# Kernel tuning notes

Hardware: AMD Instinct MI355X
Metric: run time of the kernel (lower is better)

## Reference

```python
import jax, jax.numpy as jnp
import numpy as np

B, N = 2, 65536
GX, GY, NH = 480, 360, 32          # grid_size
FEA_DIM, OUT_DIM, MAX_PT = 9, 512, 256
HW = GX * GY


def setup_inputs() -> dict:
    key = jax.random.key(0)
    ks = jax.random.split(key, 24)
    def rn(k, shape, scale):
        return jax.random.normal(k, shape, jnp.float32) * scale
    d = {}
    d['pt_fea'] = jax.random.normal(ks[0], (B, N, FEA_DIM), jnp.float32)
    d['xy_ind'] = jax.random.randint(ks[1], (B, N, 2), 0, 360)
    # eval-mode BatchNorm1d folded into per-channel scale/shift
    for i, c in enumerate([FEA_DIM, 64, 128, 256]):
        d[f's{i}'] = 1.0 + rn(ks[2 + 2 * i], (c,), 0.05)
        d[f't{i}'] = rn(ks[3 + 2 * i], (c,), 0.05)
    for i, (cin, cout) in enumerate([(FEA_DIM, 64), (64, 128), (128, 256), (256, OUT_DIM)], 1):
        d[f'W{i}'] = rn(ks[9 + 2 * i], (cin, cout), 1.0 / np.sqrt(cin))
        d[f'b{i}'] = rn(ks[10 + 2 * i], (cout,), 0.02)
    d['Wc'] = rn(ks[20], (OUT_DIM, NH), 1.0 / np.sqrt(OUT_DIM))
    d['bc'] = rn(ks[21], (NH,), 0.02)
    return d


def _ranks(lin):
    # within-voxel rank of each point (== grp_range_torch(...)[argsort(argsort(unq_inv))])
    n = lin.shape[0]
    order = jnp.argsort(lin, stable=True)
    sl = lin[order]
    start = jnp.concatenate([jnp.ones((1,), bool), sl[1:] != sl[:-1]])
    idx = jnp.arange(n)
    run_start = jax.lax.associative_scan(jnp.maximum, jnp.where(start, idx, 0))
    return jnp.zeros(n, lin.dtype).at[order].set(idx - run_start)


def reference(pt_fea, xy_ind, s0, t0, s1, t1, s2, t2, s3, t3,
              W1, b1, W2, b2, W3, b3, W4, b4, Wc, bc):
    lin = xy_ind[..., 0] * GY + xy_ind[..., 1]          # [B,N] linear voxel id
    ranks = jax.vmap(_ranks)(lin)
    keep = ranks < MAX_PT                               # cap points per voxel
    # Simplified_PointNet: BN -> Lin -> BN -> ReLU -> ... -> Lin (eval-mode BN)
    x = pt_fea * s0 + t0
    x = jnp.maximum((x @ W1 + b1) * s1 + t1, 0.0)
    x = jnp.maximum((x @ W2 + b2) * s2 + t2, 0.0)
    x = jnp.maximum((x @ W3 + b3) * s3 + t3, 0.0)
    x = x @ W4 + b4                                     # [B,N,512]

    def pool(feat, seg, kp):
        masked = jnp.where(kp[:, None], feat, -jnp.inf)
        mx = jax.ops.segment_max(masked, seg, num_segments=HW)      # [HW,512]
        occ = jax.ops.segment_sum(jnp.ones_like(seg, jnp.float32), seg,
                                  num_segments=HW) > 0
        mx = jnp.where(occ[:, None], mx, 0.0)
        comp = jnp.maximum(mx @ Wc + bc, 0.0)           # fea_compression
        return jnp.where(occ[:, None], comp, 0.0)       # empty voxels stay 0

    grid = jax.vmap(pool)(x, lin, keep)                 # [B,HW,32]
    grid = grid.reshape(B, GX, GY, NH)
    return jnp.transpose(grid, (0, 3, 1, 2))            # to_cnn: [B,32,480,360]
```

## Files before the change

### kernel.cpp

```cpp
#include <hip/hip_runtime.h>
#include <cstdint>
#include <cstddef>

#define B_   2
#define N_   65536
#define GXv  480
#define GYv  360
#define NHv  32
#define HWv  (GXv*GYv)

typedef __attribute__((ext_vector_type(8))) short short8;
typedef __attribute__((ext_vector_type(8))) unsigned short ushort8;
typedef __attribute__((ext_vector_type(4))) float floatx4;

__device__ __forceinline__ unsigned short f2bf(float f) {
    unsigned u = __float_as_uint(f);
    u += 0x7FFFu + ((u >> 16) & 1u);
    return (unsigned short)(u >> 16);
}
__device__ __forceinline__ unsigned bf2key2(unsigned d) {
    unsigned sgn = (d >> 15) & 0x00010001u;
    return d ^ (0x80008000u | (sgn * 0x7FFFu));
}
__device__ __forceinline__ unsigned key2bf2(unsigned k) {
    unsigned sgn = (k >> 15) & 0x00010001u;
    return k ^ (0xFFFFFFFFu - sgn * 0x7FFFu);
}

__global__ void k_init_head(int* head) {
    int i = blockIdx.x * 256 + threadIdx.x;
    if (i < B_ * HWv) head[i] = -1;
}

__global__ void k_chain(const int* __restrict__ xy, int* head, int* nxt) {
    int i = blockIdx.x * 256 + threadIdx.x;
    if (i >= B_ * N_) return;
    int b = i >> 16;
    int x = xy[2 * i], y = xy[2 * i + 1];
    nxt[i] = atomicExch(&head[b * HWv + x * GYv + y], i);
}

__global__ void k_cvtB(const float* __restrict__ W, unsigned short* __restrict__ dst,
                       int K, int N) {
    int d = blockIdx.x * 256 + threadIdx.x;
    if (d >= (K * N) / 8) return;
    int l = d & 63;
    int g = d >> 6;
    int NT = N >> 4;
    int kc = g / NT, nt = g - kc * NT;
    int k0 = kc * 32 + (l >> 4) * 8, n = nt * 16 + (l & 15);
    __align__(16) unsigned short o[8];
    #pragma unroll
    for (int j = 0; j < 8; ++j) o[j] = f2bf(W[(size_t)(k0 + j) * N + n]);
    *reinterpret_cast<uint4*>(dst + (size_t)d * 8) = *reinterpret_cast<const uint4*>(o);
}

__global__ __launch_bounds__(256, 3) void k_mlp(
        const float* __restrict__ pt_fea,
        const float* __restrict__ s0v, const float* __restrict__ t0v,
        const float* __restrict__ s1v, const float* __restrict__ t1v,
        const float* __restrict__ s2v, const float* __restrict__ t2v,
        const float* __restrict__ s3v, const float* __restrict__ t3v,
        const float* __restrict__ W1, const float* __restrict__ b1,
        const unsigned short* __restrict__ W2B, const float* __restrict__ b2,
        const unsigned short* __restrict__ W3B, const float* __restrict__ b3,
        const unsigned short* __restrict__ W4B, const float* __restrict__ b4,
        unsigned short* __restrict__ x4out)
{
    __shared__ __align__(16) char smem[49152];
    unsigned short* x1A = (unsigned short*)smem;
    unsigned short* x3A = (unsigned short*)smem;
    unsigned short* x2A = (unsigned short*)(smem + 32768);
    float*          x0s = (float*)(smem + 32768);
    unsigned short* rep = (unsigned short*)(smem + 32768);

    const short8* W2v = reinterpret_cast<const short8*>(W2B);
    const short8* W3v = reinterpret_cast<const short8*>(W3B);
    const short8* W4v = reinterpret_cast<const short8*>(W4B);

    int tid = threadIdx.x;
    int w = tid >> 6, lane = tid & 63;
    int bid = blockIdx.x;
    int b = bid >> 10, n0 = (bid & 1023) << 6;
    const float* fea = pt_fea + ((size_t)(b * N_ + n0)) * 9;

    for (int idx = tid; idx < 576; idx += 256) {
        int kk = idx % 9;
        x0s[idx] = fea[idx] * s0v[kk] + t0v[kk];
    }
    short8 b2r[2][2];
    #pragma unroll
    for (int kc = 0; kc < 2; ++kc)
        #pragma unroll
        for (int t = 0; t < 2; ++t)
            b2r[kc][t] = W2v[(kc * 8 + w * 2 + t) * 64 + lane];
    __syncthreads();

    {
        int p = tid & 63, q = tid >> 6;
        float a0[9];
        #pragma unroll
        for (int k = 0; k < 9; ++k) a0[k] = x0s[p * 9 + k];
        float acc1[16];
        #pragma unroll
        for (int c = 0; c < 16; ++c) acc1[c] = 0.f;
        #pragma unroll
        for (int k = 0; k < 9; ++k) {
            #pragma unroll
            for (int c4 = 0; c4 < 4; ++c4) {
                float4 wv = *reinterpret_cast<const float4*>(&W1[k * 64 + q * 16 + c4 * 4]);
                acc1[c4*4+0] = fmaf(a0[k], wv.x, acc1[c4*4+0]);
                acc1[c4*4+1] = fmaf(a0[k], wv.y, acc1[c4*4+1]);
                acc1[c4*4+2] = fmaf(a0[k], wv.z, acc1[c4*4+2]);
                acc1[c4*4+3] = fmaf(a0[k], wv.w, acc1[c4*4+3]);
            }
        }
        #pragma unroll
        for (int h = 0; h < 2; ++h) {
            __align__(16) unsigned short o[8];
            #pragma unroll
            for (int j = 0; j < 8; ++j) {
                int c = q * 16 + h * 8 + j;
                o[j] = f2bf(fmaxf(fmaf(acc1[h * 8 + j] + b1[c], s1v[c], t1v[c]), 0.f));
            }
            int lane2 = (p & 15) + (((q & 1) * 2 + h) << 4);
            *reinterpret_cast<uint4*>(x1A + (((p >> 4) * 2 + (q >> 1)) * 64 + lane2) * 8) =
                *reinterpret_cast<const uint4*>(o);
        }
    }
    __syncthreads();

    {
        floatx4 acc2[4][2];
        #pragma unroll
        for (int mt = 0; mt < 4; ++mt)
            #pragma unroll
            for (int nt = 0; nt < 2; ++nt) acc2[mt][nt] = (floatx4)0.f;
        #pragma unroll
        for (int kc = 0; kc < 2; ++kc) {
            short8 a[4];
            #pragma unroll
            for (int mt = 0; mt < 4; ++mt)
                a[mt] = *reinterpret_cast<const short8*>(x1A + ((mt * 2 + kc) * 64 + lane) * 8);
            #pragma unroll
            for (int nt = 0; nt < 2; ++nt)
                #pragma unroll
                for (int mt = 0; mt < 4; ++mt)
                    acc2[mt][nt] = __builtin_amdgcn_mfma_f32_16x16x32_bf16(
                        a[mt], b2r[kc][nt], acc2[mt][nt], 0, 0, 0);
        }
        #pragma unroll
        for (int nt = 0; nt < 2; ++nt) {
            int c = (w * 2 + nt) * 16 + (lane & 15);
            float bb = b2[c], sc = s2v[c], tt = t2v[c];
            #pragma unroll
            for (int mt = 0; mt < 4; ++mt)
                #pragma unroll
                for (int r = 0; r < 4; ++r) {
                    int ml = (lane >> 4) * 4 + r;
                    float v = fmaxf(fmaf(acc2[mt][nt][r] + bb, sc, tt), 0.f);
                    x2A[((mt * 4 + (c >> 5)) * 64 + ml + (((c >> 3) & 3) << 4)) * 8 + (c & 7)] = f2bf(v);
                }
        }
    }
    short8 bb3[3][4];
    #pragma unroll
    for (int t = 0; t < 4; ++t) bb3[0][t] = W3v[(w * 4 + t) * 64 + lane];
    #pragma unroll
    for (int t = 0; t < 4; ++t) bb3[1][t] = W3v[(16 + w * 4 + t) * 64 + lane];
    __syncthreads();

    {
        floatx4 acc3[4][4];
        #pragma unroll
        for (int mt = 0; mt < 4; ++mt)
            #pragma unroll
            for (int nt = 0; nt < 4; ++nt) acc3[mt][nt] = (floatx4)0.f;
        #pragma unroll
        for (int kc = 0; kc < 4; ++kc) {
            if (kc + 2 < 4) {
                #pragma unroll
                for (int t = 0; t < 4; ++t)
                    bb3[(kc + 2) % 3][t] = W3v[((kc + 2) * 16 + w * 4 + t) * 64 + lane];
            }
            short8 a[4];
            #pragma unroll
            for (int mt = 0; mt < 4; ++mt)
                a[mt] = *reinterpret_cast<const short8*>(x2A + ((mt * 4 + kc) * 64 + lane) * 8);
            #pragma unroll
            for (int nt = 0; nt < 4; ++nt)
                #pragma unroll
                for (int mt = 0; mt < 4; ++mt)
                    acc3[mt][nt] = __builtin_amdgcn_mfma_f32_16x16x32_bf16(
                        a[mt], bb3[kc % 3][nt], acc3[mt][nt], 0, 0, 0);
        }
        #pragma unroll
        for (int nt = 0; nt < 4; ++nt) {
            int c = w * 64 + nt * 16 + (lane & 15);
            float bb = b3[c], sc = s3v[c], tt = t3v[c];
            #pragma unroll
            for (int mt = 0; mt < 4; ++mt)
                #pragma unroll
                for (int r = 0; r < 4; ++r) {
                    int ml = (lane >> 4) * 4 + r;
                    float v = fmaxf(fmaf(acc3[mt][nt][r] + bb, sc, tt), 0.f);
                    x3A[((mt * 8 + (c >> 5)) * 64 + ml + (((c >> 3) & 3) << 4)) * 8 + (c & 7)] = f2bf(v);
                }
        }
    }
    short8 bb4[3][4];
    #pragma unroll
    for (int t = 0; t < 4; ++t) bb4[0][t] = W4v[(w * 4 + t) * 64 + lane];
    #pragma unroll
    for (int t = 0; t < 4; ++t) bb4[1][t] = W4v[(32 + w * 4 + t) * 64 + lane];
    __syncthreads();

    #pragma unroll
    for (int nh = 0; nh < 2; ++nh) {
        floatx4 acc4[4][4];
        #pragma unroll
        for (int mt = 0; mt < 4; ++mt)
            #pragma unroll
            for (int nt = 0; nt < 4; ++nt) acc4[mt][nt] = (floatx4)0.f;
        #pragma unroll
        for (int kc = 0; kc < 8; ++kc) {
            const int g = nh * 8 + kc;
            if (g + 2 < 16) {
                const int g2 = g + 2, nh2 = g2 >> 3, kc2 = g2 & 7;
                #pragma unroll
                for (int t = 0; t < 4; ++t)
                    bb4[g2 % 3][t] = W4v[(kc2 * 32 + nh2 * 16 + w * 4 + t) * 64 + lane];
            }
            short8 a[4];
            #pragma unroll
            for (int mt = 0; mt < 4; ++mt)
                a[mt] = *reinterpret_cast<const short8*>(x3A + ((mt * 8 + kc) * 64 + lane) * 8);
            #pragma unroll
            for (int nt = 0; nt < 4; ++nt)
                #pragma unroll
                for (int mt = 0; mt < 4; ++mt)
                    acc4[mt][nt] = __builtin_amdgcn_mfma_f32_16x16x32_bf16(
                        a[mt], bb4[g % 3][nt], acc4[mt][nt], 0, 0, 0);
        }
        #pragma unroll
        for (int mh = 0; mh < 2; ++mh) {
            #pragma unroll
            for (int nt = 0; nt < 4; ++nt) {
                int cl = w * 64 + nt * 16 + (lane & 15);
                float bb = b4[nh * 256 + cl];
                #pragma unroll
                for (int mt2 = 0; mt2 < 2; ++mt2) {
                    #pragma unroll
                    for (int r = 0; r < 4; ++r) {
                        int ml = mt2 * 16 + (lane >> 4) * 4 + r;
                        rep[ml * 256 + cl] = f2bf(acc4[mh * 2 + mt2][nt][r] + bb);
                    }
                }
            }
            __syncthreads();
            #pragma unroll
            for (int r2 = 0; r2 < 4; ++r2) {
                int q = r2 * 256 + tid;
                int m = q >> 5, co = (q & 31) * 8;
                uint4 v = *reinterpret_cast<const uint4*>(rep + m * 256 + co);
                v.x = bf2key2(v.x); v.y = bf2key2(v.y);
                v.z = bf2key2(v.z); v.w = bf2key2(v.w);
                *reinterpret_cast<uint4*>(
                    &x4out[((size_t)(b * N_ + n0 + mh * 32 + m)) * 512 + nh * 256 + co]) = v;
            }
            __syncthreads();
        }
    }
}

__global__ __launch_bounds__(256) void k_pool(
        const int* __restrict__ head, const int* __restrict__ nxt,
        const unsigned short* __restrict__ x4,
        const unsigned short* __restrict__ WcB, const float* __restrict__ bcv,
        float* __restrict__ out)
{
    __shared__ __align__(16) unsigned short mxA[16 * 64 * 8];
    __shared__ float part[4][16 * 17];
    __shared__ int occ[16];
    int tid = threadIdx.x;
    int w = tid >> 6, lane = tid & 63;
    int kh = w >> 1, ntw = w & 1;
    int g = tid >> 4, l = tid & 15;
    int s = blockIdx.x;
    int half = s & 1, sx2 = s >> 1;
    int b = sx2 / GXv, x = sx2 - b * GXv;
    int ybase = half * 192;
    int ntiles = half ? 11 : 12;
    const int* hrow = head + (size_t)b * HWv + (size_t)x * GYv;

    short8 breg[8];
    #pragma unroll
    for (int kk = 0; kk < 8; ++kk)
        breg[kk] = *reinterpret_cast<const short8*>(
            WcB + (size_t)(((kh * 8 + kk) * 2 + ntw) * 64 + lane) * 8);

    #pragma unroll 1
    for (int t = 0; t < ntiles; ++t) {
        int y0 = ybase + t * 16;
        {
            int y = y0 + g;
            int h = (y < GYv) ? hrow[y] : -1;
            if (l == 0) occ[g] = h;
            ushort8 mx[4];
            if (h >= 0) {
                #pragma unroll
                for (int i = 0; i < 4; ++i) mx[i] = (ushort8)((unsigned short)0x007F);
                int cur = h;
                while (cur >= 0) {
                    const ushort8* row = reinterpret_cast<const ushort8*>(x4 + (size_t)cur * 512);
                    ushort8 r0 = row[0 * 16 + l];
                    ushort8 r1 = row[1 * 16 + l];
                    ushort8 r2 = row[2 * 16 + l];
                    ushort8 r3 = row[3 * 16 + l];
                    mx[0] = __builtin_elementwise_max(mx[0], r0);
                    mx[1] = __builtin_elementwise_max(mx[1], r1);
                    mx[2] = __builtin_elementwise_max(mx[2], r2);
                    mx[3] = __builtin_elementwise_max(mx[3], r3);
                    cur = nxt[cur];
                }
            } else {
                #pragma unroll
                for (int i = 0; i < 4; ++i) mx[i] = (ushort8)((unsigned short)0x8000);
            }
            #pragma unroll
            for (int i = 0; i < 4; ++i) {
                uint4 v = *reinterpret_cast<uint4*>(&mx[i]);
                v.x = key2bf2(v.x); v.y = key2bf2(v.y);
                v.z = key2bf2(v.z); v.w = key2bf2(v.w);
                int kc = i * 4 + (l >> 2);
                int dl = g | ((l & 3) << 4);
                int dls = dl ^ (((kc & 3) << 2) | ((dl >> 4) & 3));
                *reinterpret_cast<uint4*>(&mxA[(kc * 64 + dls) * 8]) = v;
            }
        }
        __syncthreads();
        {
            floatx4 acc = (floatx4)0.f;
            #pragma unroll
            for (int kk = 0; kk < 8; ++kk) {
                int kk2 = kh * 8 + kk;
                int dls = lane ^ (((kk2 & 3) << 2) | ((lane >> 4) & 3));
                short8 a = *reinterpret_cast<const short8*>(&mxA[(kk2 * 64 + dls) * 8]);
                acc = __builtin_amdgcn_mfma_f32_16x16x32_bf16(a, breg[kk], acc, 0, 0, 0);
            }
            #pragma unroll
            for (int r = 0; r < 4; ++r)
                part[w][((lane >> 4) * 4 + r) * 17 + (lane & 15)] = acc[r];
        }
        __syncthreads();
        {
            int m = tid & 15, n = tid >> 4;
            int y = y0 + m;
            if (y < GYv) {
                bool o = occ[m] >= 0;
                float v0 = o ? fmaxf(part[0][m * 17 + n] + part[2][m * 17 + n] + bcv[n], 0.f) : 0.f;
                float v1 = o ? fmaxf(part[1][m * 17 + n] + part[3][m * 17 + n] + bcv[n + 16], 0.f) : 0.f;
                out[(((size_t)b * NHv + n)      * GXv + x) * GYv + y] = v0;
                out[(((size_t)b * NHv + n + 16) * GXv + x) * GYv + y] = v1;
            }
        }
        __syncthreads();
    }
}

extern "C" void kernel_launch(void* const* d_in, const int* in_sizes, int n_in,
                              void* d_out, int out_size, void* d_ws, size_t ws_size,
                              hipStream_t stream) {
    const float* pt_fea = (const float*)d_in[0];
    const int*   xy     = (const int*)d_in[1];
    const float* s0v = (const float*)d_in[2];  const float* t0v = (const float*)d_in[3];
    const float* s1v = (const float*)d_in[4];  const float* t1v = (const float*)d_in[5];
    const float* s2v = (const float*)d_in[6];  const float* t2v = (const float*)d_in[7];
    const float* s3v = (const float*)d_in[8];  const float* t3v = (const float*)d_in[9];
    const float* W1  = (const float*)d_in[10]; const float* b1  = (const float*)d_in[11];
    const float* W2  = (const float*)d_in[12]; const float* b2  = (const float*)d_in[13];
    const float* W3  = (const float*)d_in[14]; const float* b3  = (const float*)d_in[15];
    const float* W4  = (const float*)d_in[16]; const float* b4  = (const float*)d_in[17];
    const float* Wc  = (const float*)d_in[18]; const float* bc  = (const float*)d_in[19];

    char* ws = (char*)d_ws;
    size_t off = 0;
    unsigned short* x4   = (unsigned short*)(ws + off); off += (size_t)B_ * N_ * 512 * 2;
    int* head            = (int*)(ws + off);            off += (size_t)B_ * HWv * 4;
    int* nxt             = (int*)(ws + off);            off += (size_t)B_ * N_ * 4;
    unsigned short* W2B  = (unsigned short*)(ws + off); off += 64 * 128 * 2;
    unsigned short* W3B  = (unsigned short*)(ws + off); off += 128 * 256 * 2;
    unsigned short* W4B  = (unsigned short*)(ws + off); off += 256 * 512 * 2;
    unsigned short* WcB  = (unsigned short*)(ws + off); off += 512 * 32 * 2;

    hipLaunchKernelGGL(k_init_head, dim3(1350), dim3(256), 0, stream, head);
    hipLaunchKernelGGL(k_chain,     dim3(512),  dim3(256), 0, stream, xy, head, nxt);
    hipLaunchKernelGGL(k_cvtB,      dim3(4),    dim3(256), 0, stream, W2, W2B, 64, 128);
    hipLaunchKernelGGL(k_cvtB,      dim3(16),   dim3(256), 0, stream, W3, W3B, 128, 256);
    hipLaunchKernelGGL(k_cvtB,      dim3(64),   dim3(256), 0, stream, W4, W4B, 256, 512);
    hipLaunchKernelGGL(k_cvtB,      dim3(8),    dim3(256), 0, stream, Wc, WcB, 512, 32);
    hipLaunchKernelGGL(k_mlp,       dim3(2048), dim3(256), 0, stream,
        pt_fea, s0v, t0v, s1v, t1v, s2v, t2v, s3v, t3v,
        W1, b1, W2B, b2, W3B, b3, W4B, b4, x4);
    hipLaunchKernelGGL(k_pool,      dim3(1920), dim3(256), 0, stream,
        head, nxt, x4, WcB, bc, (float*)d_out);
}
```

Baseline: 145.2 us.

## Raise wave priority around MFMA loops and merge final output staging

Wraps every MFMA inner loop, in the MLP kernel and in the pool kernel, with s_setprio(1)/s_setprio(0) so matrix-issuing waves get scheduling priority over waves doing memory or epilogue work. For the second half of layer 4, the output tile is staged through the full 32 KB region holding x3A, which is dead after the last MFMA, so all 64 rows are written with one barrier pair instead of two. The first half keeps the two-pass staging. The risk is that the priority hints change little or starve other waves, and the bigger staging region adds an extra barrier before it is reused.

```diff
diff --git a/kernel.cpp b/kernel.cpp
--- a/kernel.cpp
+++ b/kernel.cpp
@@ -73,6 +73,7 @@
     unsigned short* x2A = (unsigned short*)(smem + 32768);
     float*          x0s = (float*)(smem + 32768);
     unsigned short* rep = (unsigned short*)(smem + 32768);
+    unsigned short* rep32 = (unsigned short*)smem;
 
     const short8* W2v = reinterpret_cast<const short8*>(W2B);
     const short8* W3v = reinterpret_cast<const short8*>(W3B);
@@ -136,6 +137,7 @@
         for (int mt = 0; mt < 4; ++mt)
             #pragma unroll
             for (int nt = 0; nt < 2; ++nt) acc2[mt][nt] = (floatx4)0.f;
+        __builtin_amdgcn_s_setprio(1);
         #pragma unroll
         for (int kc = 0; kc < 2; ++kc) {
             short8 a[4];
@@ -149,6 +151,7 @@
                     acc2[mt][nt] = __builtin_amdgcn_mfma_f32_16x16x32_bf16(
                         a[mt], b2r[kc][nt], acc2[mt][nt], 0, 0, 0);
         }
+        __builtin_amdgcn_s_setprio(0);
         #pragma unroll
         for (int nt = 0; nt < 2; ++nt) {
             int c = (w * 2 + nt) * 16 + (lane & 15);
@@ -176,6 +179,7 @@
         for (int mt = 0; mt < 4; ++mt)
             #pragma unroll
             for (int nt = 0; nt < 4; ++nt) acc3[mt][nt] = (floatx4)0.f;
+        __builtin_amdgcn_s_setprio(1);
         #pragma unroll
         for (int kc = 0; kc < 4; ++kc) {
             if (kc + 2 < 4) {
@@ -194,6 +198,7 @@
                     acc3[mt][nt] = __builtin_amdgcn_mfma_f32_16x16x32_bf16(
                         a[mt], bb3[kc % 3][nt], acc3[mt][nt], 0, 0, 0);
         }
+        __builtin_amdgcn_s_setprio(0);
         #pragma unroll
         for (int nt = 0; nt < 4; ++nt) {
             int c = w * 64 + nt * 16 + (lane & 15);
@@ -222,6 +227,7 @@
         for (int mt = 0; mt < 4; ++mt)
             #pragma unroll
             for (int nt = 0; nt < 4; ++nt) acc4[mt][nt] = (floatx4)0.f;
+        __builtin_amdgcn_s_setprio(1);
         #pragma unroll
         for (int kc = 0; kc < 8; ++kc) {
             const int g = nh * 8 + kc;
@@ -242,33 +248,61 @@
                     acc4[mt][nt] = __builtin_amdgcn_mfma_f32_16x16x32_bf16(
                         a[mt], bb4[g % 3][nt], acc4[mt][nt], 0, 0, 0);
         }
-        #pragma unroll
-        for (int mh = 0; mh < 2; ++mh) {
+        __builtin_amdgcn_s_setprio(0);
+        unsigned short* orow = x4out + ((size_t)(b * N_ + n0)) * 512 + nh * 256;
+        if (nh == 0) {
+            #pragma unroll
+            for (int mh = 0; mh < 2; ++mh) {
+                #pragma unroll
+                for (int nt = 0; nt < 4; ++nt) {
+                    int cl = w * 64 + nt * 16 + (lane & 15);
+                    float bb = b4[cl];
+                    #pragma unroll
+                    for (int mt2 = 0; mt2 < 2; ++mt2) {
+                        #pragma unroll
+                        for (int r = 0; r < 4; ++r) {
+                            int ml = mt2 * 16 + (lane >> 4) * 4 + r;
+                            rep[ml * 256 + cl] = f2bf(acc4[mh * 2 + mt2][nt][r] + bb);
+                        }
+                    }
+                }
+                __syncthreads();
+                #pragma unroll
+                for (int r2 = 0; r2 < 4; ++r2) {
+                    int q = r2 * 256 + tid;
+                    int m = q >> 5, co = (q & 31) * 8;
+                    uint4 v = *reinterpret_cast<const uint4*>(rep + m * 256 + co);
+                    v.x = bf2key2(v.x); v.y = bf2key2(v.y);
+                    v.z = bf2key2(v.z); v.w = bf2key2(v.w);
+                    *reinterpret_cast<uint4*>(
+                        &orow[((size_t)(mh * 32 + m)) * 512 + co]) = v;
+                }
+                __syncthreads();
+            }
+        } else {
+            __syncthreads();
             #pragma unroll
             for (int nt = 0; nt < 4; ++nt) {
                 int cl = w * 64 + nt * 16 + (lane & 15);
-                float bb = b4[nh * 256 + cl];
-                #pragma unroll
-                for (int mt2 = 0; mt2 < 2; ++mt2) {
+                float bb = b4[256 + cl];
+                #pragma unroll
+                for (int mt = 0; mt < 4; ++mt)
                     #pragma unroll
                     for (int r = 0; r < 4; ++r) {
-                        int ml = mt2 * 16 + (lane >> 4) * 4 + r;
-                        rep[ml * 256 + cl] = f2bf(acc4[mh * 2 + mt2][nt][r] + bb);
+                        int m = mt * 16 + (lane >> 4) * 4 + r;
+                        rep32[m * 256 + cl] = f2bf(acc4[mt][nt][r] + bb);
                     }
-                }
             }
             __syncthreads();
             #pragma unroll
-            for (int r2 = 0; r2 < 4; ++r2) {
+            for (int r2 = 0; r2 < 8; ++r2) {
                 int q = r2 * 256 + tid;
                 int m = q >> 5, co = (q & 31) * 8;
-                uint4 v = *reinterpret_cast<const uint4*>(rep + m * 256 + co);
+                uint4 v = *reinterpret_cast<const uint4*>(rep32 + m * 256 + co);
                 v.x = bf2key2(v.x); v.y = bf2key2(v.y);
                 v.z = bf2key2(v.z); v.w = bf2key2(v.w);
-                *reinterpret_cast<uint4*>(
-                    &x4out[((size_t)(b * N_ + n0 + mh * 32 + m)) * 512 + nh * 256 + co]) = v;
-            }
-            __syncthreads();
+                *reinterpret_cast<uint4*>(&orow[(size_t)m * 512 + co]) = v;
+            }
         }
     }
 }
@@ -341,6 +375,7 @@
         __syncthreads();
         {
             floatx4 acc = (floatx4)0.f;
+            __builtin_amdgcn_s_setprio(1);
             #pragma unroll
             for (int kk = 0; kk < 8; ++kk) {
                 int kk2 = kh * 8 + kk;
@@ -348,6 +383,7 @@
                 short8 a = *reinterpret_cast<const short8*>(&mxA[(kk2 * 64 + dls) * 8]);
                 acc = __builtin_amdgcn_mfma_f32_16x16x32_bf16(a, breg[kk], acc, 0, 0, 0);
             }
+            __builtin_amdgcn_s_setprio(0);
             #pragma unroll
             for (int r = 0; r < 4; ++r)
                 part[w][((lane >> 4) * 4 + r) * 17 + (lane & 15)] = acc[r];
```

New measurement: 146.7 us. No clear change (+1.0%).
